# Kernel tuning notes

Hardware: AMD Instinct MI355X
Metric: run time of the kernel (lower is better)

The kernel has to match this reference:

```python
import jax, jax.numpy as jnp
import numpy as np

EPS = 1e-8

def setup_inputs() -> dict:
    key = jax.random.key(0)
    k1, k2, k3 = jax.random.split(key, 3)
    B, N, M = 4, 8192, 8192
    source = jax.random.normal(k1, (B, N, 3), dtype=jnp.float32)
    target = jax.random.normal(k2, (B, M, 3), dtype=jnp.float32)
    weights = jax.random.uniform(k3, (B, N), dtype=jnp.float32)
    return {"source": source, "target": target, "weights": weights}

def reference(source, target, weights):
    # Pairwise squared distances: (B, N, M)
    diff = source[:, :, None, :] - target[:, None, :, :]
    sq_distances = jnp.sum(diff * diff, axis=-1)
    # squared=False -> take sqrt with eps for stability
    distances = jnp.sqrt(sq_distances + EPS)
    # source -> target nearest-neighbor distance, weighted
    s2t = jnp.min(distances, axis=2) * weights  # (B, N)
    forward_loss = jnp.mean(s2t)
    # symmetric=True: target -> source (unweighted, as in original)
    t2s = jnp.min(distances, axis=1)  # (B, M)
    backward_loss = jnp.mean(t2s)
    return forward_loss + backward_loss
```

## Files before the change

### kernel.cpp

```cpp
#include <hip/hip_runtime.h>
#include <math.h>


#define EPS 1e-8f

typedef _Float16 f16x8 __attribute__((ext_vector_type(8)));
typedef float    f32x16 __attribute__((ext_vector_type(16)));

constexpr int B_    = 4;
constexpr int N_    = 8192;
constexpr int TPB   = 256;
constexpr int QPW   = 64;
constexpr int QPB   = 4 * QPW;
constexpr int RCH   = 8;
constexpr int CHUNK = N_ / RCH;
constexpr int RB    = 64;

__global__ __launch_bounds__(TPB, 6)
void nn_mfma_kernel(const float* __restrict__ src, const float* __restrict__ tgt,
                    unsigned int* __restrict__ minA, unsigned int* __restrict__ minB)
{
    __shared__ f16x8 sref[CHUNK + 64];

    const int zb  = blockIdx.z;
    const int dir = zb >> 2;
    const int b   = zb & 3;
    const float* Rraw = (dir ? src : tgt) + ((size_t)b * N_ + (size_t)blockIdx.y * CHUNK) * 3;
    const float* Qraw = (dir ? tgt : src) + (size_t)b * N_ * 3;
    unsigned int* omin = (dir ? minB : minA) + (size_t)b * N_;

    const int tid = threadIdx.x;
    const _Float16 h0 = (_Float16)0.f;
    const _Float16 h1 = (_Float16)1.f;

    for (int k = tid; k < CHUNK; k += TPB) {
        const float* rp = Rraw + (size_t)k * 3;
        _Float16 hx = (_Float16)rp[0], hy = (_Float16)rp[1], hz = (_Float16)rp[2];
        float fx = (float)hx, fy = (float)hy, fz = (float)hz;
        float rsq = fx * fx + fy * fy + fz * fz;
        _Float16 rh = (_Float16)rsq;
        _Float16 rl = (_Float16)(rsq - (float)rh);
        f16x8 a = {(_Float16)(-2.f * fx), (_Float16)(-2.f * fy),
                   (_Float16)(-2.f * fz), rh, rl, h0, h0, h0};
        sref[k] = a;
    }
    if (tid < 64) {
        f16x8 z = {h0, h0, h0, h0, h0, h0, h0, h0};
        sref[CHUNK + tid] = z;
    }

    const int lane = tid & 63;
    const int wv   = tid >> 6;
    const int l31  = lane & 31;
    const int half = lane >> 5;
    const int qb   = blockIdx.x * QPB + wv * QPW;

    f16x8 B0 = {h0, h0, h0, h0, h0, h0, h0, h0};
    f16x8 B1 = B0;
    float qs0 = 0.f, qs1 = 0.f;
    if (half == 0) {
        const float* q0 = Qraw + (size_t)(qb + l31) * 3;
        const float* q1 = Qraw + (size_t)(qb + 32 + l31) * 3;
        _Float16 ax = (_Float16)q0[0], ay = (_Float16)q0[1], az = (_Float16)q0[2];
        _Float16 bx = (_Float16)q1[0], by = (_Float16)q1[1], bz = (_Float16)q1[2];
        float fax = (float)ax, fay = (float)ay, faz = (float)az;
        float fbx = (float)bx, fby = (float)by, fbz = (float)bz;
        B0 = f16x8{ax, ay, az, h1, h1, h0, h0, h0};
        B1 = f16x8{bx, by, bz, h1, h1, h0, h0, h0};
        qs0 = fax * fax + fay * fay + faz * faz;
        qs1 = fbx * fbx + fby * fby + fbz * fbz;
    }
    __syncthreads();

    f32x16 zc;
#pragma unroll
    for (int i = 0; i < 16; ++i) zc[i] = 0.f;

    int idx = (half == 0) ? l31 : CHUNK;
    const int step = (half == 0) ? 32 : 0;
    float mn0a = 3.0e38f, mn0b = 3.0e38f, mn1a = 3.0e38f, mn1b = 3.0e38f;

    f16x8 a = sref[idx];
    idx += step;
    for (int s = 0; s < CHUNK / 32; ++s) {
        f16x8 an = sref[idx];
        idx += step;
        f32x16 d0 = __builtin_amdgcn_mfma_f32_32x32x16_f16(a, B0, zc, 0, 0, 0);
        f32x16 d1 = __builtin_amdgcn_mfma_f32_32x32x16_f16(a, B1, zc, 0, 0, 0);
#pragma unroll
        for (int r = 0; r < 8; r += 2) {
            mn0a = fminf(fminf(d0[r], d0[r + 1]), mn0a);
            mn1a = fminf(fminf(d1[r], d1[r + 1]), mn1a);
        }
#pragma unroll
        for (int r = 8; r < 16; r += 2) {
            mn0b = fminf(fminf(d0[r], d0[r + 1]), mn0b);
            mn1b = fminf(fminf(d1[r], d1[r + 1]), mn1b);
        }
        a = an;
    }

    float mn0 = fminf(mn0a, mn0b);
    float mn1 = fminf(mn1a, mn1b);
    mn0 = fminf(mn0, __shfl_xor(mn0, 32));
    mn1 = fminf(mn1, __shfl_xor(mn1, 32));
    if (half == 0) {
        atomicMin(&omin[qb + l31],      __float_as_uint(fmaxf(mn0 + qs0, 0.f)));
        atomicMin(&omin[qb + 32 + l31], __float_as_uint(fmaxf(mn1 + qs1, 0.f)));
    }
}

__global__ __launch_bounds__(TPB)
void reduce_kernel(const unsigned int* __restrict__ minA,
                   const unsigned int* __restrict__ minB,
                   const float* __restrict__ w,
                   float* __restrict__ out)
{
    const int BN = B_ * N_;
    const float invBN = 1.0f / (float)BN;

    float sum = 0.0f;
    for (int t = blockIdx.x * TPB + threadIdx.x; t < BN; t += RB * TPB) {
        sum += sqrtf(__uint_as_float(minA[t]) + EPS) * w[t];
        sum += sqrtf(__uint_as_float(minB[t]) + EPS);
    }
    sum *= invBN;

    __shared__ float ss[TPB / 64];
    int lane = threadIdx.x & 63;
    int wid  = threadIdx.x >> 6;
#pragma unroll
    for (int off = 32; off > 0; off >>= 1) sum += __shfl_down(sum, off);
    if (lane == 0) ss[wid] = sum;
    __syncthreads();
    if (threadIdx.x == 0) {
        float s = 0.0f;
#pragma unroll
        for (int i = 0; i < TPB / 64; ++i) s += ss[i];
        atomicAdd(out, s);
    }
}

extern "C" void kernel_launch(void* const* d_in, const int* in_sizes, int n_in,
                              void* d_out, int out_size, void* d_ws, size_t ws_size,
                              hipStream_t stream)
{
    const float* src = (const float*)d_in[0];
    const float* tgt = (const float*)d_in[1];
    const float* w   = (const float*)d_in[2];
    float* out = (float*)d_out;

    const size_t BN = (size_t)B_ * N_;
    unsigned int* minA = (unsigned int*)d_ws;
    unsigned int* minB = minA + BN;

    hipMemsetAsync(minA, 0x7F, 2 * BN * sizeof(unsigned int), stream);
    hipMemsetAsync(out, 0, sizeof(float), stream);

    dim3 grid(N_ / QPB, RCH, 2 * B_);
    nn_mfma_kernel<<<grid, TPB, 0, stream>>>(src, tgt, minA, minB);

    reduce_kernel<<<RB, TPB, 0, stream>>>(minA, minB, w, out);
}
```

Before: 76.75 us.

## Fuse distance reduction into the NN kernel and loop over all reference chunks per block

```diff
diff --git a/kernel.cpp b/kernel.cpp
--- a/kernel.cpp
+++ b/kernel.cpp
@@ -9,135 +9,151 @@
 
 constexpr int B_    = 4;
 constexpr int N_    = 8192;
-constexpr int TPB   = 256;
+constexpr int TPB   = 128;
 constexpr int QPW   = 64;
-constexpr int QPB   = 4 * QPW;
-constexpr int RCH   = 8;
-constexpr int CHUNK = N_ / RCH;
-constexpr int RB    = 64;
+constexpr int QPB   = 2 * QPW;
+constexpr int CHUNK = 2048;
+constexpr int NCH   = N_ / CHUNK;
+constexpr int NF    = CHUNK / 32;
+constexpr int RPT   = CHUNK / TPB;
+constexpr int QBLK  = N_ / QPB;
+constexpr int NBLK  = QBLK * 2 * B_;
 
-__global__ __launch_bounds__(TPB, 6)
-void nn_mfma_kernel(const float* __restrict__ src, const float* __restrict__ tgt,
-                    unsigned int* __restrict__ minA, unsigned int* __restrict__ minB)
+#define FOLD(d, ma, mb)                                         \
+    _Pragma("unroll")                                           \
+    for (int r = 0; r < 8; r += 2)                              \
+        ma = fminf(fminf(d[r], d[r + 1]), ma);                  \
+    _Pragma("unroll")                                           \
+    for (int r = 8; r < 16; r += 2)                             \
+        mb = fminf(fminf(d[r], d[r + 1]), mb);
+
+__global__ __launch_bounds__(TPB, 1)
+void nn_fused_kernel(const float* __restrict__ src, const float* __restrict__ tgt,
+                     const float* __restrict__ w, float* __restrict__ bpart)
 {
-    __shared__ f16x8 sref[CHUNK + 64];
+    __shared__ f16x8 sref[CHUNK];
+    __shared__ float ss[TPB / 64];
 
-    const int zb  = blockIdx.z;
+    const int zb  = blockIdx.y;
     const int dir = zb >> 2;
     const int b   = zb & 3;
-    const float* Rraw = (dir ? src : tgt) + ((size_t)b * N_ + (size_t)blockIdx.y * CHUNK) * 3;
+    const float* Rraw = (dir ? src : tgt) + (size_t)b * N_ * 3;
     const float* Qraw = (dir ? tgt : src) + (size_t)b * N_ * 3;
-    unsigned int* omin = (dir ? minB : minA) + (size_t)b * N_;
 
-    const int tid = threadIdx.x;
-    const _Float16 h0 = (_Float16)0.f;
-    const _Float16 h1 = (_Float16)1.f;
-
-    for (int k = tid; k < CHUNK; k += TPB) {
-        const float* rp = Rraw + (size_t)k * 3;
-        _Float16 hx = (_Float16)rp[0], hy = (_Float16)rp[1], hz = (_Float16)rp[2];
-        float fx = (float)hx, fy = (float)hy, fz = (float)hz;
-        float rsq = fx * fx + fy * fy + fz * fz;
-        _Float16 rh = (_Float16)rsq;
-        _Float16 rl = (_Float16)(rsq - (float)rh);
-        f16x8 a = {(_Float16)(-2.f * fx), (_Float16)(-2.f * fy),
-                   (_Float16)(-2.f * fz), rh, rl, h0, h0, h0};
-        sref[k] = a;
-    }
-    if (tid < 64) {
-        f16x8 z = {h0, h0, h0, h0, h0, h0, h0, h0};
-        sref[CHUNK + tid] = z;
-    }
-
+    const int tid  = threadIdx.x;
     const int lane = tid & 63;
     const int wv   = tid >> 6;
     const int l31  = lane & 31;
     const int half = lane >> 5;
     const int qb   = blockIdx.x * QPB + wv * QPW;
 
+    const _Float16 h0 = (_Float16)0.f;
+    const _Float16 h1 = (_Float16)1.f;
+
     f16x8 B0 = {h0, h0, h0, h0, h0, h0, h0, h0};
     f16x8 B1 = B0;
-    float qs0 = 0.f, qs1 = 0.f;
-    if (half == 0) {
+    float qs0, qs1;
+    {
         const float* q0 = Qraw + (size_t)(qb + l31) * 3;
         const float* q1 = Qraw + (size_t)(qb + 32 + l31) * 3;
         _Float16 ax = (_Float16)q0[0], ay = (_Float16)q0[1], az = (_Float16)q0[2];
         _Float16 bx = (_Float16)q1[0], by = (_Float16)q1[1], bz = (_Float16)q1[2];
         float fax = (float)ax, fay = (float)ay, faz = (float)az;
         float fbx = (float)bx, fby = (float)by, fbz = (float)bz;
-        B0 = f16x8{ax, ay, az, h1, h1, h0, h0, h0};
-        B1 = f16x8{bx, by, bz, h1, h1, h0, h0, h0};
         qs0 = fax * fax + fay * fay + faz * faz;
         qs1 = fbx * fbx + fby * fby + fbz * fbz;
+        if (half == 0) {
+            B0 = f16x8{ax, ay, az, h1, h1, h0, h0, h0};
+            B1 = f16x8{bx, by, bz, h1, h1, h0, h0, h0};
+        }
     }
-    __syncthreads();
 
-    f32x16 zc;
+    float rx[RPT], ry[RPT], rz[RPT];
 #pragma unroll
-    for (int i = 0; i < 16; ++i) zc[i] = 0.f;
+    for (int i = 0; i < RPT; ++i) {
+        const float* rp = Rraw + (size_t)(i * TPB + tid) * 3;
+        rx[i] = rp[0]; ry[i] = rp[1]; rz[i] = rp[2];
+    }
 
-    int idx = (half == 0) ? l31 : CHUNK;
-    const int step = (half == 0) ? 32 : 0;
+    const f32x16 zc = {};
     float mn0a = 3.0e38f, mn0b = 3.0e38f, mn1a = 3.0e38f, mn1b = 3.0e38f;
 
-    f16x8 a = sref[idx];
-    idx += step;
-    for (int s = 0; s < CHUNK / 32; ++s) {
-        f16x8 an = sref[idx];
-        idx += step;
-        f32x16 d0 = __builtin_amdgcn_mfma_f32_32x32x16_f16(a, B0, zc, 0, 0, 0);
-        f32x16 d1 = __builtin_amdgcn_mfma_f32_32x32x16_f16(a, B1, zc, 0, 0, 0);
+    for (int c = 0; c < NCH; ++c) {
+        __syncthreads();
 #pragma unroll
-        for (int r = 0; r < 8; r += 2) {
-            mn0a = fminf(fminf(d0[r], d0[r + 1]), mn0a);
-            mn1a = fminf(fminf(d1[r], d1[r + 1]), mn1a);
+        for (int i = 0; i < RPT; ++i) {
+            _Float16 hx = (_Float16)rx[i], hy = (_Float16)ry[i], hz = (_Float16)rz[i];
+            float fx = (float)hx, fy = (float)hy, fz = (float)hz;
+            float rsq = fx * fx + fy * fy + fz * fz;
+            _Float16 rh = (_Float16)rsq;
+            _Float16 rl = (_Float16)(rsq - (float)rh);
+            sref[i * TPB + tid] = f16x8{(_Float16)(-2.f * fx), (_Float16)(-2.f * fy),
+                                        (_Float16)(-2.f * fz), rh, rl, h0, h0, h0};
         }
+        __syncthreads();
+        if (c + 1 < NCH) {
+            const float* Rc = Rraw + (size_t)(c + 1) * CHUNK * 3;
 #pragma unroll
-        for (int r = 8; r < 16; r += 2) {
-            mn0b = fminf(fminf(d0[r], d0[r + 1]), mn0b);
-            mn1b = fminf(fminf(d1[r], d1[r + 1]), mn1b);
+            for (int i = 0; i < RPT; ++i) {
+                const float* rp = Rc + (size_t)(i * TPB + tid) * 3;
+                rx[i] = rp[0]; ry[i] = rp[1]; rz[i] = rp[2];
+            }
         }
-        a = an;
+
+        f16x8 A0 = sref[l31];
+        f16x8 Ax = sref[32 + l31];
+        f16x8 Ay = sref[64 + l31];
+        f32x16 dP0 = __builtin_amdgcn_mfma_f32_32x32x16_f16(A0, B0, zc, 0, 0, 0);
+        f32x16 dP1 = __builtin_amdgcn_mfma_f32_32x32x16_f16(A0, B1, zc, 0, 0, 0);
+#pragma unroll
+        for (int f = 1; f < NF; ++f) {
+            f32x16 dC0 = __builtin_amdgcn_mfma_f32_32x32x16_f16(Ax, B0, zc, 0, 0, 0);
+            f32x16 dC1 = __builtin_amdgcn_mfma_f32_32x32x16_f16(Ax, B1, zc, 0, 0, 0);
+            f16x8 An = (f + 2 < NF) ? sref[(f + 2) * 32 + l31] : Ay;
+            FOLD(dP0, mn0a, mn0b)
+            FOLD(dP1, mn1a, mn1b)
+            dP0 = dC0; dP1 = dC1;
+            Ax = Ay; Ay = An;
+        }
+        FOLD(dP0, mn0a, mn0b)
+        FOLD(dP1, mn1a, mn1b)
     }
 
     float mn0 = fminf(mn0a, mn0b);
     float mn1 = fminf(mn1a, mn1b);
     mn0 = fminf(mn0, __shfl_xor(mn0, 32));
     mn1 = fminf(mn1, __shfl_xor(mn1, 32));
-    if (half == 0) {
-        atomicMin(&omin[qb + l31],      __float_as_uint(fmaxf(mn0 + qs0, 0.f)));
-        atomicMin(&omin[qb + 32 + l31], __float_as_uint(fmaxf(mn1 + qs1, 0.f)));
+    float d0 = sqrtf(fmaxf(mn0 + qs0, 0.f) + EPS);
+    float d1 = sqrtf(fmaxf(mn1 + qs1, 0.f) + EPS);
+    float sl;
+    if (dir == 0) {
+        const float* wb = w + (size_t)b * N_;
+        sl = d0 * wb[qb + l31] + d1 * wb[qb + 32 + l31];
+    } else {
+        sl = d0 + d1;
     }
+#pragma unroll
+    for (int off = 32; off > 0; off >>= 1) sl += __shfl_down(sl, off);
+    if (lane == 0) ss[wv] = sl;
+    __syncthreads();
+    if (tid == 0) bpart[blockIdx.y * QBLK + blockIdx.x] = ss[0] + ss[1];
 }
 
-__global__ __launch_bounds__(TPB)
-void reduce_kernel(const unsigned int* __restrict__ minA,
-                   const unsigned int* __restrict__ minB,
-                   const float* __restrict__ w,
-                   float* __restrict__ out)
+__global__ __launch_bounds__(NBLK)
+void reduce2_kernel(const float* __restrict__ bpart, float* __restrict__ out)
 {
-    const int BN = B_ * N_;
-    const float invBN = 1.0f / (float)BN;
-
-    float sum = 0.0f;
-    for (int t = blockIdx.x * TPB + threadIdx.x; t < BN; t += RB * TPB) {
-        sum += sqrtf(__uint_as_float(minA[t]) + EPS) * w[t];
-        sum += sqrtf(__uint_as_float(minB[t]) + EPS);
-    }
-    sum *= invBN;
-
-    __shared__ float ss[TPB / 64];
-    int lane = threadIdx.x & 63;
-    int wid  = threadIdx.x >> 6;
+    __shared__ float ss[NBLK / 64];
+    float v = bpart[threadIdx.x];
 #pragma unroll
-    for (int off = 32; off > 0; off >>= 1) sum += __shfl_down(sum, off);
-    if (lane == 0) ss[wid] = sum;
+    for (int off = 32; off > 0; off >>= 1) v += __shfl_down(v, off);
+    int lane = threadIdx.x & 63, wid = threadIdx.x >> 6;
+    if (lane == 0) ss[wid] = v;
     __syncthreads();
     if (threadIdx.x == 0) {
-        float s = 0.0f;
+        float s = 0.f;
 #pragma unroll
-        for (int i = 0; i < TPB / 64; ++i) s += ss[i];
-        atomicAdd(out, s);
+        for (int i = 0; i < NBLK / 64; ++i) s += ss[i];
+        out[0] = s * 0.5f / (float)(B_ * N_);
     }
 }
 
@@ -150,15 +166,9 @@
     const float* w   = (const float*)d_in[2];
     float* out = (float*)d_out;
 
-    const size_t BN = (size_t)B_ * N_;
-    unsigned int* minA = (unsigned int*)d_ws;
-    unsigned int* minB = minA + BN;
+    float* bpart = (float*)d_ws;
 
-    hipMemsetAsync(minA, 0x7F, 2 * BN * sizeof(unsigned int), stream);
-    hipMemsetAsync(out, 0, sizeof(float), stream);
-
-    dim3 grid(N_ / QPB, RCH, 2 * B_);
-    nn_mfma_kernel<<<grid, TPB, 0, stream>>>(src, tgt, minA, minB);
-
-    reduce_kernel<<<RB, TPB, 0, stream>>>(minA, minB, w, out);
+    dim3 grid(QBLK, 2 * B_);
+    nn_fused_kernel<<<grid, TPB, 0, stream>>>(src, tgt, w, bpart);
+    reduce2_kernel<<<1, NBLK, 0, stream>>>(bpart, out);
 }
```

Measured after the change: 105.4 us. 37.3% more time.
